# Kernel optimization log

Hardware: AMD Instinct MI355X
Metric: run time of the kernel (lower is better)

## Reference

```python
import jax, jax.numpy as jnp
import numpy as np

N = 50000      # number of nodes (rows of edge_embeddings)
E = 800000     # number of edges
D = 256        # edge_dim
TOPK = 50


def setup_inputs() -> dict:
    key = jax.random.key(0)
    k1, k2, k3, k4, k5, k6 = jax.random.split(key, 6)
    edge_embeddings = jax.random.normal(k1, (N, D), dtype=jnp.float32)
    edge_index = jax.random.randint(k2, (2, E), 0, N, dtype=jnp.int64)
    # PyTorch nn.Linear default init: U(-1/sqrt(fan_in), 1/sqrt(fan_in))
    s1 = 1.0 / np.sqrt(2 * D)
    s2 = 1.0 / np.sqrt(D)
    W1 = jax.random.uniform(k3, (2 * D, D), jnp.float32, -s1, s1)
    b1 = jax.random.uniform(k4, (D,), jnp.float32, -s1, s1)
    W2 = jax.random.uniform(k5, (D, 1), jnp.float32, -s2, s2)
    b2 = jax.random.uniform(k6, (1,), jnp.float32, -s2, s2)
    return {"edge_embeddings": edge_embeddings, "W1": W1, "b1": b1,
            "W2": W2, "b2": b2, "edge_index": edge_index, "top_k": TOPK}


def reference(edge_embeddings, W1, b1, W2, b2, edge_index, top_k):
    src, dst = edge_index[0], edge_index[1]           # [E]
    valid = src < dst                                  # original keeps only i<j pairs
    # gather + concat: [E, 2D]
    pair_emb = jnp.concatenate([edge_embeddings[src], edge_embeddings[dst]], axis=-1)
    h = jax.nn.relu(pair_emb @ W1 + b1)                # [E, D]
    score = jax.nn.sigmoid(h @ W2 + b2)[:, 0]          # [E], in (0,1)
    # invalid edges get score -1 (< any sigmoid output) so topk picks only valid ones
    masked = jnp.where(valid, score, jnp.float32(-1.0))
    top_scores, top_idx = jax.lax.top_k(masked, top_k)
    top_pairs = edge_index[:, top_idx]                 # [2, k] (src,dst) of top edges
    return top_pairs, top_scores
```

## Files before the change

### kernel.cpp

```cpp
#include <hip/hip_runtime.h>
#include <hip/hip_bf16.h>
#include <cstdint>

#define TOPK 50
#define CANDS 400
#define HIST_BINS 16384
#define CAND_CAP 16384
#define NFBLK 512
#define SORT_CAP 8192

typedef __attribute__((ext_vector_type(8))) short bf16x8;
typedef __attribute__((ext_vector_type(4))) float f32x4;

__device__ __forceinline__ unsigned short f2bf(float f) {
    unsigned u = __float_as_uint(f);
    u += 0x7FFFu + ((u >> 16) & 1u);
    return (unsigned short)(u >> 16);
}

__global__ __launch_bounds__(256) void prep_kernel(const float* __restrict__ W1,
                                                   unsigned* __restrict__ Wcf4,
                                                   unsigned* __restrict__ hist,
                                                   unsigned* __restrict__ misc,
                                                   const int* __restrict__ eidx) {
    int g = blockIdx.x * blockDim.x + threadIdx.x;
    {
        int l = g & 63;
        int kt = (g >> 6) & 7;
        int nt = g >> 9;
        int col = nt * 16 + (l & 15);
        int kb = kt * 32 + (l >> 4) * 8;
        unsigned short h[8];
#pragma unroll
        for (int j = 0; j < 8; ++j) {
            int k = kb + j;
            float f = (col < 256) ? W1[k * 256 + col] : W1[(256 + k) * 256 + (col - 256)];
            h[j] = f2bf(f);
        }
        unsigned* dst = Wcf4 + (size_t)g * 4;
        dst[0] = (unsigned)h[0] | ((unsigned)h[1] << 16);
        dst[1] = (unsigned)h[2] | ((unsigned)h[3] << 16);
        dst[2] = (unsigned)h[4] | ((unsigned)h[5] << 16);
        dst[3] = (unsigned)h[6] | ((unsigned)h[7] << 16);
    }
    if (g < HIST_BINS) hist[g] = 0;
    if (g == 0) {
        int allz = 1;
        for (int q = 0; q < 64; ++q)
            if (eidx[2 * q + 1] != 0) { allz = 0; break; }
        misc[0] = (unsigned)allz;
        misc[2] = 0;
        misc[3] = 0;
        misc[4] = 0;
    }
}

__global__ __launch_bounds__(256) void gemm_fused(const float* __restrict__ emb,
                                                  const bf16x8* __restrict__ Bv,
                                                  const float* __restrict__ b1,
                                                  unsigned char* __restrict__ C8, int M) {
    __shared__ uint4 afrag[2048];
    const int t = threadIdx.x;
    const int w = t >> 6;
    const int l = t & 63;

    uint2* w2 = (uint2*)afrag;
#pragma unroll
    for (int iter = 0; iter < 16; ++iter) {
        int r = iter * 4 + w;
        int c0 = l * 4;
        int gr = blockIdx.x * 64 + r;
        float4 v = make_float4(0.f, 0.f, 0.f, 0.f);
        if (gr < M) v = *(const float4*)&emb[(size_t)gr * 256 + c0];
        unsigned u0 = (unsigned)f2bf(v.x) | ((unsigned)f2bf(v.y) << 16);
        unsigned u1 = (unsigned)f2bf(v.z) | ((unsigned)f2bf(v.w) << 16);
        int mt = r >> 4;
        int kt = c0 >> 5;
        int lane = (r & 15) + ((c0 & 31) >> 3) * 16;
        int f = mt * 8 + kt;
        int slot = f * 64 + (lane ^ (f & 7));
        w2[slot * 2 + ((c0 & 7) >> 2)] = make_uint2(u0, u1);
    }
    __syncthreads();

    const int wn = w;
#pragma unroll
    for (int nh = 0; nh < 2; ++nh) {
        f32x4 acc[4][4];
#pragma unroll
        for (int i = 0; i < 4; ++i)
#pragma unroll
            for (int j = 0; j < 4; ++j) acc[i][j] = (f32x4){0.f, 0.f, 0.f, 0.f};

        const int nt0 = wn * 8 + nh * 4;
        bf16x8 bcur[4];
#pragma unroll
        for (int j = 0; j < 4; ++j)
            bcur[j] = Bv[(size_t)((nt0 + j) * 8 + 0) * 64 + l];

#pragma unroll
        for (int kt = 0; kt < 8; ++kt) {
            bf16x8 af[4];
#pragma unroll
            for (int i = 0; i < 4; ++i)
                af[i] = *(const bf16x8*)&afrag[(i * 8 + kt) * 64 + (l ^ kt)];
            bf16x8 bnxt[4];
            if (kt < 7) {
#pragma unroll
                for (int j = 0; j < 4; ++j)
                    bnxt[j] = Bv[(size_t)((nt0 + j) * 8 + kt + 1) * 64 + l];
            }
#pragma unroll
            for (int i = 0; i < 4; ++i)
#pragma unroll
                for (int j = 0; j < 4; ++j)
                    acc[i][j] = __builtin_amdgcn_mfma_f32_16x16x32_bf16(af[i], bcur[j], acc[i][j], 0, 0, 0);
            if (kt < 7) {
#pragma unroll
                for (int j = 0; j < 4; ++j) bcur[j] = bnxt[j];
            }
        }

#pragma unroll
        for (int i = 0; i < 4; ++i) {
            int row0 = blockIdx.x * 64 + i * 16 + (l >> 4) * 4;
#pragma unroll
            for (int j = 0; j < 4; ++j) {
                int col = (nt0 + j) * 16 + (l & 15);
                float bias = (col < 256) ? b1[col] : 0.f;
#pragma unroll
                for (int r = 0; r < 4; ++r) {
                    float v = acc[i][j][r] + bias;
                    int pk = __builtin_amdgcn_cvt_pk_fp8_f32(v, v, 0, false);
                    C8[(size_t)(row0 + r) * 512 + col] = (unsigned char)(pk & 0xFF);
                }
            }
        }
    }
}

__global__ __launch_bounds__(256) void count_valid(const int* __restrict__ eidx,
                                                   const unsigned* __restrict__ misc,
                                                   unsigned* __restrict__ bcount, int E) {
    const int is64 = (int)misc[0];
    const int chunk = (E + gridDim.x - 1) / gridDim.x;
    const int lo = blockIdx.x * chunk;
    const int hi = min(E, lo + chunk);
    unsigned cnt = 0;
    for (int e = lo + threadIdx.x; e < hi; e += blockDim.x) {
        int s, d;
        if (is64) {
            s = ((const int2*)eidx)[e].x;
            d = ((const int2*)eidx)[(size_t)e + E].x;
        } else {
            s = eidx[e];
            d = eidx[e + E];
        }
        cnt += (s < d);
    }
#pragma unroll
    for (int off = 32; off; off >>= 1) cnt += __shfl_xor(cnt, off, 64);
    __shared__ unsigned wsum[4];
    if ((threadIdx.x & 63) == 0) wsum[threadIdx.x >> 6] = cnt;
    __syncthreads();
    if (threadIdx.x == 0)
        bcount[blockIdx.x] = wsum[0] + wsum[1] + wsum[2] + wsum[3];
}

__global__ __launch_bounds__(256) void write_valid_scan(const int* __restrict__ eidx,
                                                        unsigned* __restrict__ misc,
                                                        const unsigned* __restrict__ bcount,
                                                        int* __restrict__ vsrc,
                                                        int* __restrict__ vdst,
                                                        int* __restrict__ vid, int E) {
    const int is64 = (int)misc[0];
    const int bid = blockIdx.x;
    const int t = threadIdx.x;
    __shared__ unsigned red[256];

    unsigned c0 = bcount[t], c1 = bcount[t + 256];
    unsigned pa = ((t < bid) ? c0 : 0u) + ((t + 256 < bid) ? c1 : 0u);
    red[t] = pa;
    __syncthreads();
    for (int s = 128; s; s >>= 1) {
        if (t < s) red[t] += red[t + s];
        __syncthreads();
    }
    const unsigned myoff = red[0];
    __syncthreads();
    red[t] = c0 + c1;
    __syncthreads();
    for (int s = 128; s; s >>= 1) {
        if (t < s) red[t] += red[t + s];
        __syncthreads();
    }
    if (bid == 0 && t == 0) misc[4] = red[0];

    const int chunk = (E + gridDim.x - 1) / gridDim.x;
    const int lo = bid * chunk;
    const int hi = min(E, lo + chunk);
    const int lane = t & 63;
    const int w = t >> 6;
    __shared__ unsigned wcnt[4];
    unsigned running = myoff;
    for (int base = lo; base < hi; base += blockDim.x) {
        int e = base + t;
        bool valid = false;
        int s = 0, d = 0;
        if (e < hi) {
            if (is64) {
                s = ((const int2*)eidx)[e].x;
                d = ((const int2*)eidx)[(size_t)e + E].x;
            } else {
                s = eidx[e];
                d = eidx[e + E];
            }
            valid = s < d;
        }
        unsigned long long m = __ballot(valid);
        unsigned pfx = __popcll(m & ((1ull << lane) - 1ull));
        if (lane == 0) wcnt[w] = __popcll(m);
        __syncthreads();
        unsigned wbase = running;
        for (int i = 0; i < w; ++i) wbase += wcnt[i];
        if (valid) {
            unsigned p = wbase + pfx;
            vsrc[p] = s;
            vdst[p] = d;
            vid[p] = e;
        }
        unsigned tot = wcnt[0] + wcnt[1] + wcnt[2] + wcnt[3];
        __syncthreads();
        running += tot;
    }
}

__device__ __forceinline__ float dotq(unsigned a, unsigned b, float4 w) {
    float s;
    s  = fmaxf(__builtin_amdgcn_cvt_f32_fp8(a, 0) + __builtin_amdgcn_cvt_f32_fp8(b, 0), 0.f) * w.x;
    s += fmaxf(__builtin_amdgcn_cvt_f32_fp8(a, 1) + __builtin_amdgcn_cvt_f32_fp8(b, 1), 0.f) * w.y;
    s += fmaxf(__builtin_amdgcn_cvt_f32_fp8(a, 2) + __builtin_amdgcn_cvt_f32_fp8(b, 2), 0.f) * w.z;
    s += fmaxf(__builtin_amdgcn_cvt_f32_fp8(a, 3) + __builtin_amdgcn_cvt_f32_fp8(b, 3), 0.f) * w.w;
    return s;
}

__global__ __launch_bounds__(256) void edge_score_fp8(const unsigned char* __restrict__ C8,
                                                      const int* __restrict__ vsrc,
                                                      const int* __restrict__ vdst,
                                                      const float* __restrict__ W2,
                                                      const float* __restrict__ b2,
                                                      float* __restrict__ svals,
                                                      const unsigned* __restrict__ misc) {
    const int V = (int)misc[4];
    const int lane = threadIdx.x & 63;
    const int q = lane & 15;
    const int g = lane >> 4;
    const int wid = blockIdx.x * (blockDim.x >> 6) + (threadIdx.x >> 6);
    const int nw = gridDim.x * (blockDim.x >> 6);

    const float4 w0 = *(const float4*)&W2[q * 16 + 0];
    const float4 w1 = *(const float4*)&W2[q * 16 + 4];
    const float4 w2 = *(const float4*)&W2[q * 16 + 8];
    const float4 w3 = *(const float4*)&W2[q * 16 + 12];
    const float bb2 = b2[0];

    for (int base = wid * 4; base < V; base += nw * 4) {
        const int slot = base + g;
        const bool ok = slot < V;
        const int src = ok ? vsrc[slot] : 0;
        const int dst = ok ? vdst[slot] : 0;
        const uint4 ua = *(const uint4*)(C8 + (size_t)src * 512 + q * 16);
        const uint4 ub = *(const uint4*)(C8 + (size_t)dst * 512 + 256 + q * 16);
        float p = dotq(ua.x, ub.x, w0);
        p += dotq(ua.y, ub.y, w1);
        p += dotq(ua.z, ub.z, w2);
        p += dotq(ua.w, ub.w, w3);
        p += __shfl_xor(p, 1, 64);
        p += __shfl_xor(p, 2, 64);
        p += __shfl_xor(p, 4, 64);
        p += __shfl_xor(p, 8, 64);
        if (q == 0 && ok) {
            float z = p + bb2;
            float sc = 1.0f / (1.0f + expf(-z));
            svals[slot] = sc;
        }
    }
}

__global__ __launch_bounds__(256) void hist_kernel(const float* __restrict__ svals,
                                                   const unsigned* __restrict__ misc,
                                                   unsigned* __restrict__ hist) {
    __shared__ unsigned lh[HIST_BINS];
    const int V = (int)misc[4];
    const int t = threadIdx.x;
    for (int i = t; i < HIST_BINS; i += 256) lh[i] = 0;
    __syncthreads();
    int i = blockIdx.x * blockDim.x + t;
    int stride = gridDim.x * blockDim.x;
    for (int v = i; v < V; v += stride)
        atomicAdd(&lh[__float_as_uint(svals[v]) >> 16], 1u);
    __syncthreads();
    for (int b = t; b < HIST_BINS; b += 256) {
        unsigned c = lh[b];
        if (c) atomicAdd(&hist[b], c);
    }
}

__global__ void scan_hist(const unsigned* __restrict__ hist, unsigned* __restrict__ misc) {
    __shared__ unsigned chunk[256];
    int t = threadIdx.x;
    unsigned s = 0;
    for (int i = 0; i < 64; ++i) s += hist[t * 64 + i];
    chunk[t] = s;
    __syncthreads();
    if (t == 0) {
        unsigned cum = 0;
        int c;
        unsigned thr = 0;
        for (c = 255; c >= 0; --c) {
            if (cum + chunk[c] >= CANDS) break;
            cum += chunk[c];
        }
        if (c >= 0) {
            for (int b = c * 64 + 63; b >= c * 64; --b) {
                cum += hist[b];
                if (cum >= CANDS) { thr = ((unsigned)b) << 16; break; }
            }
        }
        misc[2] = thr;
    }
}

__global__ void compact(const float* __restrict__ svals, const int* __restrict__ vid,
                        unsigned* __restrict__ misc,
                        unsigned long long* __restrict__ cand) {
    const int V = (int)misc[4];
    const unsigned thr = misc[2];
    int i = blockIdx.x * blockDim.x + threadIdx.x;
    int stride = gridDim.x * blockDim.x;
    for (int v = i; v < V; v += stride) {
        unsigned bits = __float_as_uint(svals[v]);
        if (bits >= thr) {
            unsigned pos = atomicAdd(&misc[3], 1u);
            if (pos < CAND_CAP)
                cand[pos] = ((unsigned long long)bits << 32) |
                            (unsigned)(0xFFFFFFFFu - (unsigned)vid[v]);
        }
    }
}

__global__ __launch_bounds__(256) void rescore(const float* __restrict__ emb,
                                               const float* __restrict__ W1,
                                               const float* __restrict__ b1,
                                               const float* __restrict__ W2,
                                               const float* __restrict__ b2,
                                               const int* __restrict__ eidx,
                                               const unsigned long long* __restrict__ cand,
                                               const unsigned* __restrict__ misc,
                                               unsigned long long* __restrict__ rescored,
                                               int E) {
    __shared__ float es[256], ed[256];
    __shared__ float red[256];
    const int C = (int)min(misc[3], (unsigned)CAND_CAP);
    const int is64 = (int)misc[0];
    const int t = threadIdx.x;
    for (int c = blockIdx.x; c < C; c += gridDim.x) {
        unsigned long long entry = cand[c];
        unsigned e = 0xFFFFFFFFu - (unsigned)(entry & 0xFFFFFFFFu);
        int src, dst;
        if (is64) {
            src = eidx[2 * (size_t)e];
            dst = eidx[2 * ((size_t)e + E)];
        } else {
            src = eidx[e];
            dst = eidx[e + E];
        }
        es[t] = emb[(size_t)src * 256 + t];
        ed[t] = emb[(size_t)dst * 256 + t];
        __syncthreads();
        float h = b1[t];
#pragma unroll 8
        for (int k = 0; k < 256; ++k) h += es[k] * W1[k * 256 + t];
#pragma unroll 8
        for (int k = 0; k < 256; ++k) h += ed[k] * W1[(256 + k) * 256 + t];
        red[t] = fmaxf(h, 0.f) * W2[t];
        __syncthreads();
        for (int s = 128; s; s >>= 1) {
            if (t < s) red[t] += red[t + s];
            __syncthreads();
        }
        if (t == 0) {
            float z = red[0] + b2[0];
            float sc = 1.0f / (1.0f + expf(-z));
            rescored[c] = ((unsigned long long)__float_as_uint(sc) << 32) |
                          (unsigned)(0xFFFFFFFFu - e);
        }
        __syncthreads();
    }
}

__global__ __launch_bounds__(256) void final_topk(unsigned long long* __restrict__ rescored,
                                                  const unsigned* __restrict__ misc,
                                                  const int* __restrict__ eidx,
                                                  float* __restrict__ out, int E) {
    __shared__ unsigned long long a[SORT_CAP];
    const int t = threadIdx.x;
    const int C = (int)min(misc[3], (unsigned)CAND_CAP);
    const int is64 = (int)misc[0];

    if (C <= SORT_CAP) {
        int n = 256;
        while (n < C) n <<= 1;
        for (int i = t; i < n; i += 256) a[i] = (i < C) ? rescored[i] : 0ull;
        __syncthreads();
        for (int k = 2; k <= n; k <<= 1) {
            for (int j = k >> 1; j > 0; j >>= 1) {
                for (int i = t; i < n; i += 256) {
                    int ixj = i ^ j;
                    if (ixj > i) {
                        unsigned long long x = a[i], y = a[ixj];
                        bool sw = ((i & k) == 0) ? (x < y) : (x > y);
                        if (sw) { a[i] = y; a[ixj] = x; }
                    }
                }
                __syncthreads();
            }
        }
        if (t < TOPK) {
            unsigned long long m = a[t];
            if (m != 0ull) {
                unsigned bits = (unsigned)(m >> 32);
                unsigned e = 0xFFFFFFFFu - (unsigned)(m & 0xFFFFFFFFu);
                int src, dst;
                if (is64) {
                    src = eidx[2 * (size_t)e];
                    dst = eidx[2 * ((size_t)e + E)];
                } else {
                    src = eidx[e];
                    dst = eidx[e + E];
                }
                out[t] = (float)src;
                out[TOPK + t] = (float)dst;
                out[2 * TOPK + t] = __uint_as_float(bits);
            } else {
                out[t] = -1.f;
                out[TOPK + t] = -1.f;
                out[2 * TOPK + t] = -1.f;
            }
        }
        return;
    }

    __shared__ unsigned long long red[256];
    for (int r = 0; r < TOPK; ++r) {
        unsigned long long best = 0ull;
        for (int i = t; i < C; i += 256) {
            unsigned long long v = rescored[i];
            if (v > best) best = v;
        }
        red[t] = best;
        __syncthreads();
        for (int s = 128; s; s >>= 1) {
            if (t < s) {
                if (red[t + s] > red[t]) red[t] = red[t + s];
            }
            __syncthreads();
        }
        unsigned long long m = red[0];
        __syncthreads();
        for (int i = t; i < C; i += 256)
            if (rescored[i] == m) rescored[i] = 0ull;
        if (t == 0) {
            if (m != 0ull) {
                unsigned bits = (unsigned)(m >> 32);
                unsigned e = 0xFFFFFFFFu - (unsigned)(m & 0xFFFFFFFFu);
                int src, dst;
                if (is64) {
                    src = eidx[2 * (size_t)e];
                    dst = eidx[2 * ((size_t)e + E)];
                } else {
                    src = eidx[e];
                    dst = eidx[e + E];
                }
                out[r] = (float)src;
                out[TOPK + r] = (float)dst;
                out[2 * TOPK + r] = __uint_as_float(bits);
            } else {
                out[r] = -1.f;
                out[TOPK + r] = -1.f;
                out[2 * TOPK + r] = -1.f;
            }
        }
        __syncthreads();
    }
}

extern "C" void kernel_launch(void* const* d_in, const int* in_sizes, int n_in,
                              void* d_out, int out_size, void* d_ws, size_t ws_size,
                              hipStream_t stream) {
    const float* emb = (const float*)d_in[0];
    const float* W1  = (const float*)d_in[1];
    const float* b1  = (const float*)d_in[2];
    const float* W2  = (const float*)d_in[3];
    const float* b2  = (const float*)d_in[4];
    const int*   eidx = (const int*)d_in[5];

    const int M = in_sizes[0] / 256;
    const int E = in_sizes[5] / 2;
    const int Mpad = ((M + 63) / 64) * 64;

    char* p = (char*)d_ws;
    auto alloc = [&](size_t bytes) {
        char* r = p;
        p += (bytes + 255) & ~(size_t)255;
        return r;
    };
    unsigned* Wcf4 = (unsigned*)alloc(256 * 512 * 2);
    unsigned char* C8 = (unsigned char*)alloc((size_t)Mpad * 512);
    float* svals = (float*)alloc((size_t)E * 4);
    int* vsrc = (int*)alloc((size_t)E * 4);
    int* vdst = (int*)alloc((size_t)E * 4);
    int* vid  = (int*)alloc((size_t)E * 4);
    unsigned* hist = (unsigned*)alloc(HIST_BINS * 4);
    unsigned long long* cand = (unsigned long long*)alloc(CAND_CAP * 8);
    unsigned long long* resc = (unsigned long long*)alloc(CAND_CAP * 8);
    unsigned* bcount = (unsigned*)alloc(NFBLK * 4);
    unsigned* misc = (unsigned*)alloc(256);

    float* out = (float*)d_out;

    prep_kernel<<<64, 256, 0, stream>>>(W1, Wcf4, hist, misc, eidx);

    gemm_fused<<<Mpad / 64, 256, 0, stream>>>(emb, (const bf16x8*)Wcf4, b1, C8, M);

    count_valid<<<NFBLK, 256, 0, stream>>>(eidx, misc, bcount, E);
    write_valid_scan<<<NFBLK, 256, 0, stream>>>(eidx, misc, bcount, vsrc, vdst, vid, E);

    edge_score_fp8<<<2048, 256, 0, stream>>>(C8, vsrc, vdst, W2, b2, svals, misc);

    hist_kernel<<<128, 256, 0, stream>>>(svals, misc, hist);

    scan_hist<<<1, 256, 0, stream>>>(hist, misc);

    compact<<<1024, 256, 0, stream>>>(svals, vid, misc, cand);

    rescore<<<1024, 256, 0, stream>>>(emb, W1, b1, W2, b2, eidx, cand, misc, resc, E);

    final_topk<<<1, 256, 0, stream>>>(resc, misc, eidx, out, E);
}
```

Baseline: 154.0 us.

## Drop valid-edge stream compaction and score edges directly with in-kernel masking

Removes the two-pass count/scan compaction kernels that built dense vsrc/vdst/vid arrays of valid edges. The scoring kernel now reads edge_index directly, writes -1 for invalid edges, and hist/compact skip negative scores and use the edge id directly. This eliminates two launches and the extra writes and reads of compacted arrays. In exchange, wavefront groups handling invalid edges sit idle during scoring, and svals is now written for all E edges.

```diff
diff --git a/kernel.cpp b/kernel.cpp
--- a/kernel.cpp
+++ b/kernel.cpp
@@ -6,7 +6,6 @@
 #define CANDS 400
 #define HIST_BINS 16384
 #define CAND_CAP 16384
-#define NFBLK 512
 #define SORT_CAP 8192
 
 typedef __attribute__((ext_vector_type(8))) short bf16x8;
@@ -51,7 +50,6 @@
         misc[0] = (unsigned)allz;
         misc[2] = 0;
         misc[3] = 0;
-        misc[4] = 0;
     }
 }
 
@@ -139,102 +137,6 @@
     }
 }
 
-__global__ __launch_bounds__(256) void count_valid(const int* __restrict__ eidx,
-                                                   const unsigned* __restrict__ misc,
-                                                   unsigned* __restrict__ bcount, int E) {
-    const int is64 = (int)misc[0];
-    const int chunk = (E + gridDim.x - 1) / gridDim.x;
-    const int lo = blockIdx.x * chunk;
-    const int hi = min(E, lo + chunk);
-    unsigned cnt = 0;
-    for (int e = lo + threadIdx.x; e < hi; e += blockDim.x) {
-        int s, d;
-        if (is64) {
-            s = ((const int2*)eidx)[e].x;
-            d = ((const int2*)eidx)[(size_t)e + E].x;
-        } else {
-            s = eidx[e];
-            d = eidx[e + E];
-        }
-        cnt += (s < d);
-    }
-#pragma unroll
-    for (int off = 32; off; off >>= 1) cnt += __shfl_xor(cnt, off, 64);
-    __shared__ unsigned wsum[4];
-    if ((threadIdx.x & 63) == 0) wsum[threadIdx.x >> 6] = cnt;
-    __syncthreads();
-    if (threadIdx.x == 0)
-        bcount[blockIdx.x] = wsum[0] + wsum[1] + wsum[2] + wsum[3];
-}
-
-__global__ __launch_bounds__(256) void write_valid_scan(const int* __restrict__ eidx,
-                                                        unsigned* __restrict__ misc,
-                                                        const unsigned* __restrict__ bcount,
-                                                        int* __restrict__ vsrc,
-                                                        int* __restrict__ vdst,
-                                                        int* __restrict__ vid, int E) {
-    const int is64 = (int)misc[0];
-    const int bid = blockIdx.x;
-    const int t = threadIdx.x;
-    __shared__ unsigned red[256];
-
-    unsigned c0 = bcount[t], c1 = bcount[t + 256];
-    unsigned pa = ((t < bid) ? c0 : 0u) + ((t + 256 < bid) ? c1 : 0u);
-    red[t] = pa;
-    __syncthreads();
-    for (int s = 128; s; s >>= 1) {
-        if (t < s) red[t] += red[t + s];
-        __syncthreads();
-    }
-    const unsigned myoff = red[0];
-    __syncthreads();
-    red[t] = c0 + c1;
-    __syncthreads();
-    for (int s = 128; s; s >>= 1) {
-        if (t < s) red[t] += red[t + s];
-        __syncthreads();
-    }
-    if (bid == 0 && t == 0) misc[4] = red[0];
-
-    const int chunk = (E + gridDim.x - 1) / gridDim.x;
-    const int lo = bid * chunk;
-    const int hi = min(E, lo + chunk);
-    const int lane = t & 63;
-    const int w = t >> 6;
-    __shared__ unsigned wcnt[4];
-    unsigned running = myoff;
-    for (int base = lo; base < hi; base += blockDim.x) {
-        int e = base + t;
-        bool valid = false;
-        int s = 0, d = 0;
-        if (e < hi) {
-            if (is64) {
-                s = ((const int2*)eidx)[e].x;
-                d = ((const int2*)eidx)[(size_t)e + E].x;
-            } else {
-                s = eidx[e];
-                d = eidx[e + E];
-            }
-            valid = s < d;
-        }
-        unsigned long long m = __ballot(valid);
-        unsigned pfx = __popcll(m & ((1ull << lane) - 1ull));
-        if (lane == 0) wcnt[w] = __popcll(m);
-        __syncthreads();
-        unsigned wbase = running;
-        for (int i = 0; i < w; ++i) wbase += wcnt[i];
-        if (valid) {
-            unsigned p = wbase + pfx;
-            vsrc[p] = s;
-            vdst[p] = d;
-            vid[p] = e;
-        }
-        unsigned tot = wcnt[0] + wcnt[1] + wcnt[2] + wcnt[3];
-        __syncthreads();
-        running += tot;
-    }
-}
-
 __device__ __forceinline__ float dotq(unsigned a, unsigned b, float4 w) {
     float s;
     s  = fmaxf(__builtin_amdgcn_cvt_f32_fp8(a, 0) + __builtin_amdgcn_cvt_f32_fp8(b, 0), 0.f) * w.x;
@@ -245,13 +147,13 @@
 }
 
 __global__ __launch_bounds__(256) void edge_score_fp8(const unsigned char* __restrict__ C8,
-                                                      const int* __restrict__ vsrc,
-                                                      const int* __restrict__ vdst,
+                                                      const int* __restrict__ eidx,
                                                       const float* __restrict__ W2,
                                                       const float* __restrict__ b2,
                                                       float* __restrict__ svals,
-                                                      const unsigned* __restrict__ misc) {
-    const int V = (int)misc[4];
+                                                      const unsigned* __restrict__ misc,
+                                                      int E) {
+    const int is64 = (int)misc[0];
     const int lane = threadIdx.x & 63;
     const int q = lane & 15;
     const int g = lane >> 4;
@@ -264,11 +166,21 @@
     const float4 w3 = *(const float4*)&W2[q * 16 + 12];
     const float bb2 = b2[0];
 
-    for (int base = wid * 4; base < V; base += nw * 4) {
-        const int slot = base + g;
-        const bool ok = slot < V;
-        const int src = ok ? vsrc[slot] : 0;
-        const int dst = ok ? vdst[slot] : 0;
+    for (int base = wid * 4; base < E; base += nw * 4) {
+        const int e = base + g;
+        if (e >= E) continue;
+        int src, dst;
+        if (is64) {
+            src = ((const int2*)eidx)[e].x;
+            dst = ((const int2*)eidx)[(size_t)e + E].x;
+        } else {
+            src = eidx[e];
+            dst = eidx[e + E];
+        }
+        if (src >= dst) {
+            if (q == 0) svals[e] = -1.0f;
+            continue;
+        }
         const uint4 ua = *(const uint4*)(C8 + (size_t)src * 512 + q * 16);
         const uint4 ub = *(const uint4*)(C8 + (size_t)dst * 512 + 256 + q * 16);
         float p = dotq(ua.x, ub.x, w0);
@@ -279,26 +191,26 @@
         p += __shfl_xor(p, 2, 64);
         p += __shfl_xor(p, 4, 64);
         p += __shfl_xor(p, 8, 64);
-        if (q == 0 && ok) {
+        if (q == 0) {
             float z = p + bb2;
             float sc = 1.0f / (1.0f + expf(-z));
-            svals[slot] = sc;
+            svals[e] = sc;
         }
     }
 }
 
 __global__ __launch_bounds__(256) void hist_kernel(const float* __restrict__ svals,
-                                                   const unsigned* __restrict__ misc,
-                                                   unsigned* __restrict__ hist) {
+                                                   unsigned* __restrict__ hist, int E) {
     __shared__ unsigned lh[HIST_BINS];
-    const int V = (int)misc[4];
     const int t = threadIdx.x;
     for (int i = t; i < HIST_BINS; i += 256) lh[i] = 0;
     __syncthreads();
     int i = blockIdx.x * blockDim.x + t;
     int stride = gridDim.x * blockDim.x;
-    for (int v = i; v < V; v += stride)
-        atomicAdd(&lh[__float_as_uint(svals[v]) >> 16], 1u);
+    for (int v = i; v < E; v += stride) {
+        float s = svals[v];
+        if (s >= 0.f) atomicAdd(&lh[__float_as_uint(s) >> 16], 1u);
+    }
     __syncthreads();
     for (int b = t; b < HIST_BINS; b += 256) {
         unsigned c = lh[b];
@@ -331,20 +243,21 @@
     }
 }
 
-__global__ void compact(const float* __restrict__ svals, const int* __restrict__ vid,
+__global__ void compact(const float* __restrict__ svals,
                         unsigned* __restrict__ misc,
-                        unsigned long long* __restrict__ cand) {
-    const int V = (int)misc[4];
+                        unsigned long long* __restrict__ cand, int E) {
     const unsigned thr = misc[2];
     int i = blockIdx.x * blockDim.x + threadIdx.x;
     int stride = gridDim.x * blockDim.x;
-    for (int v = i; v < V; v += stride) {
-        unsigned bits = __float_as_uint(svals[v]);
+    for (int e = i; e < E; e += stride) {
+        float s = svals[e];
+        if (s < 0.f) continue;
+        unsigned bits = __float_as_uint(s);
         if (bits >= thr) {
             unsigned pos = atomicAdd(&misc[3], 1u);
             if (pos < CAND_CAP)
                 cand[pos] = ((unsigned long long)bits << 32) |
-                            (unsigned)(0xFFFFFFFFu - (unsigned)vid[v]);
+                            (unsigned)(0xFFFFFFFFu - (unsigned)e);
         }
     }
 }
@@ -518,13 +431,9 @@
     unsigned* Wcf4 = (unsigned*)alloc(256 * 512 * 2);
     unsigned char* C8 = (unsigned char*)alloc((size_t)Mpad * 512);
     float* svals = (float*)alloc((size_t)E * 4);
-    int* vsrc = (int*)alloc((size_t)E * 4);
-    int* vdst = (int*)alloc((size_t)E * 4);
-    int* vid  = (int*)alloc((size_t)E * 4);
     unsigned* hist = (unsigned*)alloc(HIST_BINS * 4);
     unsigned long long* cand = (unsigned long long*)alloc(CAND_CAP * 8);
     unsigned long long* resc = (unsigned long long*)alloc(CAND_CAP * 8);
-    unsigned* bcount = (unsigned*)alloc(NFBLK * 4);
     unsigned* misc = (unsigned*)alloc(256);
 
     float* out = (float*)d_out;
@@ -533,16 +442,13 @@
 
     gemm_fused<<<Mpad / 64, 256, 0, stream>>>(emb, (const bf16x8*)Wcf4, b1, C8, M);
 
-    count_valid<<<NFBLK, 256, 0, stream>>>(eidx, misc, bcount, E);
-    write_valid_scan<<<NFBLK, 256, 0, stream>>>(eidx, misc, bcount, vsrc, vdst, vid, E);
-
-    edge_score_fp8<<<2048, 256, 0, stream>>>(C8, vsrc, vdst, W2, b2, svals, misc);
-
-    hist_kernel<<<128, 256, 0, stream>>>(svals, misc, hist);
+    edge_score_fp8<<<2048, 256, 0, stream>>>(C8, eidx, W2, b2, svals, misc, E);
+
+    hist_kernel<<<128, 256, 0, stream>>>(svals, hist, E);
 
     scan_hist<<<1, 256, 0, stream>>>(hist, misc);
 
-    compact<<<1024, 256, 0, stream>>>(svals, vid, misc, cand);
+    compact<<<1024, 256, 0, stream>>>(svals, misc, cand, E);
 
     rescore<<<1024, 256, 0, stream>>>(emb, W1, b1, W2, b2, eidx, cand, misc, resc, E);
 
```

New measurement: 164.7 us. +7.0%, slower.
